# Optimization experiments

Measured on AMD Instinct MI355X. Metric: run time of the kernel, lower is better.

The kernel has to match this reference:

```python
import jax, jax.numpy as jnp
import numpy as np

LN_EPS = 1e-5

def setup_inputs() -> dict:
    key = jax.random.key(0)
    ks = jax.random.split(key, 8)
    B, d, var_dim, hidden = 1024, 32, 64, 256
    in_dim = d * var_dim
    causal_vars = jax.random.normal(ks[0], (B, d, var_dim), dtype=jnp.float32)
    adj_soft = jax.random.uniform(ks[1], (d, d), dtype=jnp.float32)
    # Per-variable MLP params (stacked along leading d axis), torch-default-like init scale
    s1 = 1.0 / np.sqrt(in_dim)
    s2 = 1.0 / np.sqrt(hidden)
    W1 = jax.random.uniform(ks[2], (d, in_dim, hidden), minval=-s1, maxval=s1, dtype=jnp.float32)
    b1 = jax.random.uniform(ks[3], (d, hidden), minval=-s1, maxval=s1, dtype=jnp.float32)
    W2 = jax.random.uniform(ks[4], (d, hidden, var_dim), minval=-s2, maxval=s2, dtype=jnp.float32)
    b2 = jax.random.uniform(ks[5], (d, var_dim), minval=-s2, maxval=s2, dtype=jnp.float32)
    gamma = jnp.ones((d, var_dim), dtype=jnp.float32)
    beta = jnp.zeros((d, var_dim), dtype=jnp.float32)
    return {"causal_vars": causal_vars, "adj_soft": adj_soft, "W1": W1, "b1": b1,
            "W2": W2, "b2": b2, "gamma": gamma, "beta": beta}

def reference(causal_vars, adj_soft, W1, b1, W2, b2, gamma, beta):
    B, d, var_dim = causal_vars.shape
    # masked parent input for equation i: adj_soft[i, j] * causal_vars[b, j, :]
    # shape (B, d_eq, d_parent, var_dim) -> flatten parents: (B, d, d*var_dim)
    x = adj_soft[None, :, :, None] * causal_vars[:, None, :, :]
    x = x.reshape(B, d, d * var_dim)
    # grouped 2-layer MLP, distinct weights per variable i
    h = jnp.einsum('bik,ikh->bih', x, W1) + b1[None]
    h = jax.nn.gelu(h, approximate=False)
    y = jnp.einsum('bih,ihv->biv', h, W2) + b2[None]
    # LayerNorm over var_dim with per-variable affine params
    mu = jnp.mean(y, axis=-1, keepdims=True)
    var = jnp.var(y, axis=-1, keepdims=True)
    y = (y - mu) * jax.lax.rsqrt(var + LN_EPS)
    return y * gamma[None] + beta[None]  # (B, d, var_dim)
```

## Files before the change

kernel.cpp:

```cpp
#include <hip/hip_runtime.h>
#include <hip/hip_bf16.h>

typedef __bf16 bf16_t;
typedef __bf16 bf16x8 __attribute__((ext_vector_type(8)));
typedef float f32x4 __attribute__((ext_vector_type(4)));

#define NB 1024
#define ND 32
#define VD 64
#define NH 256
#define NK 2048

#define OFF_A    0
#define OFF_W1T  (4u*1024u*1024u)
#define OFF_W2T  (36u*1024u*1024u)

#define GLD16(gsrc, ldst) \
  __builtin_amdgcn_global_load_lds((const __attribute__((address_space(1))) void*)(gsrc), \
                                   (__attribute__((address_space(3))) void*)(ldst), 16, 0, 0)

__global__ __launch_bounds__(256) void prep_kernel(
    const float* __restrict__ cv, const float* __restrict__ adj,
    const float* __restrict__ W1, const float* __restrict__ W2,
    bf16_t* __restrict__ A, bf16_t* __restrict__ W1T, bf16_t* __restrict__ W2T)
{
  __shared__ float Ls[64 * 67];
  int bx = blockIdx.x;
  int tid = threadIdx.x;
  if (bx < 4096) {
    int i = bx >> 7;
    int rem = bx & 127;
    int k0 = (rem >> 2) * 64;
    int h0 = (rem & 3) * 64;
    float a = adj[i * 32 + (k0 >> 6)];
    int rrow = tid >> 4, c4 = (tid & 15) * 4;
#pragma unroll
    for (int p = 0; p < 4; ++p) {
      int row = p * 16 + rrow;
      const float* src = W1 + ((size_t)(i * 2048 + k0 + row)) * 256 + h0 + c4;
      float4 v = *(const float4*)src;
#pragma unroll
      for (int j = 0; j < 4; ++j) Ls[row * 67 + c4 + j] = a * ((const float*)&v)[j];
    }
    __syncthreads();
#pragma unroll
    for (int p = 0; p < 2; ++p) {
      int u = p * 256 + tid;
      int h = u >> 3, c8 = u & 7;
      bf16x8 o;
#pragma unroll
      for (int j = 0; j < 8; ++j) o[j] = (bf16_t)Ls[(c8 * 8 + j) * 67 + h];
      *(bf16x8*)(W1T + ((size_t)(i * 256 + h0 + h)) * 2048 + k0 + c8 * 8) = o;
    }
  } else if (bx < 5120) {
    int t = (bx - 4096) * 256 + tid;
    const float4* s = (const float4*)cv + (size_t)t * 2;
    float4 v0 = s[0], v1 = s[1];
    bf16x8 o;
    o[0] = (bf16_t)v0.x; o[1] = (bf16_t)v0.y; o[2] = (bf16_t)v0.z; o[3] = (bf16_t)v0.w;
    o[4] = (bf16_t)v1.x; o[5] = (bf16_t)v1.y; o[6] = (bf16_t)v1.z; o[7] = (bf16_t)v1.w;
    *(bf16x8*)(A + (size_t)t * 8) = o;
  } else {
    int t = (bx - 5120) * 256 + tid;
    int i = t >> 11;
    int rem = t & 2047;
    int h8 = rem >> 6;
    int v = rem & 63;
    const float* src = W2 + ((size_t)(i * 256 + h8 * 8)) * 64 + v;
    bf16x8 o;
#pragma unroll
    for (int r = 0; r < 8; ++r) o[r] = (bf16_t)src[(size_t)r * 64];
    *(bf16x8*)(W2T + ((size_t)(i * 64 + v)) * 256 + h8 * 8) = o;
  }
}

__global__ __launch_bounds__(1024, 4) void sem_main_kernel(
    const bf16_t* __restrict__ A, const bf16_t* __restrict__ W1T,
    const bf16_t* __restrict__ W2T,
    const float* __restrict__ b1, const float* __restrict__ b2,
    const float* __restrict__ gamma, const float* __restrict__ beta,
    float* __restrict__ out)
{
  __shared__ char smem[73728];

  int p = blockIdx.x;
  int L = (p & 7) * 32 + (p >> 3);
  int i = L >> 3;
  int brow = (L & 7) * 128;

  int tid = threadIdx.x;
  int lane = tid & 63;
  int wid = tid >> 6;
  int wr = wid >> 2;
  int wc = wid & 3;
  int lhi = lane >> 4;
  int llo = lane & 15;

  const bf16_t* W1Ti = W1T + (size_t)i * 256 * 2048;

  int srow = tid >> 2, sc4 = tid & 3;
  int scz = sc4 ^ ((srow >> 1) & 3);
  const bf16_t* bSrc = W1Ti + (size_t)srow * 2048 + scz * 8;
  const bf16_t* aSrc = A + (size_t)(brow + srow) * 2048 + scz * 8;
  int ldsW = wid * 1024;

  auto stage = [&](int b, int kt) {
    char* base = smem + b * 24576;
    if (wid < 8) GLD16(aSrc + (size_t)kt * 32, base + ldsW);
    GLD16(bSrc + (size_t)kt * 32, base + 8192 + ldsW);
  };

  int aOff[2], bOff[4];
#pragma unroll
  for (int m = 0; m < 2; ++m) {
    int row = wr * 32 + m * 16 + llo;
    aOff[m] = row * 64 + ((lhi ^ ((row >> 1) & 3)) * 16);
  }
#pragma unroll
  for (int n = 0; n < 4; ++n) {
    int row = wc * 64 + n * 16 + llo;
    bOff[n] = 8192 + row * 64 + ((lhi ^ ((row >> 1) & 3)) * 16);
  }

  f32x4 acc[2][4];
#pragma unroll
  for (int m = 0; m < 2; ++m)
#pragma unroll
    for (int n = 0; n < 4; ++n) acc[m][n] = (f32x4){0.f, 0.f, 0.f, 0.f};

  auto compute = [&](int b) {
    const char* base = smem + b * 24576;
    bf16x8 af[2], bfr[4];
#pragma unroll
    for (int m = 0; m < 2; ++m) af[m] = *(const bf16x8*)(base + aOff[m]);
#pragma unroll
    for (int n = 0; n < 4; ++n) bfr[n] = *(const bf16x8*)(base + bOff[n]);
    __builtin_amdgcn_s_setprio(1);
#pragma unroll
    for (int m = 0; m < 2; ++m)
#pragma unroll
      for (int n = 0; n < 4; ++n)
        acc[m][n] = __builtin_amdgcn_mfma_f32_16x16x32_bf16(af[m], bfr[n], acc[m][n], 0, 0, 0);
    __builtin_amdgcn_s_setprio(0);
  };

#define WAIT_OWN_TILE() do { \
    if (wid < 8) asm volatile("s_waitcnt vmcnt(2) lgkmcnt(0)" ::: "memory"); \
    else         asm volatile("s_waitcnt vmcnt(1) lgkmcnt(0)" ::: "memory"); \
  } while (0)

  asm volatile("" ::: "memory");
  stage(0, 0); stage(1, 1);
  int bc = 0, bs = 2;
  for (int t = 0; t < 62; ++t) {
    WAIT_OWN_TILE();
    __builtin_amdgcn_s_barrier();
    asm volatile("" ::: "memory");
    stage(bs, t + 2);
    compute(bc);
    bc = (bc == 2) ? 0 : bc + 1;
    bs = (bs == 2) ? 0 : bs + 1;
  }
  WAIT_OWN_TILE();
  __builtin_amdgcn_s_barrier();
  asm volatile("" ::: "memory");
  compute(2);
  asm volatile("s_waitcnt vmcnt(0) lgkmcnt(0)" ::: "memory");
  __builtin_amdgcn_s_barrier();
  asm volatile("" ::: "memory");
  compute(0);
  __syncthreads();

  bf16_t* Hs = (bf16_t*)smem;
  float bias[4];
#pragma unroll
  for (int n = 0; n < 4; ++n) bias[n] = b1[i * 256 + wc * 64 + n * 16 + llo];
#pragma unroll
  for (int m = 0; m < 2; ++m) {
#pragma unroll
    for (int n = 0; n < 4; ++n) {
      int col = wc * 64 + n * 16 + llo;
#pragma unroll
      for (int r = 0; r < 4; ++r) {
        int row = wr * 32 + m * 16 + lhi * 4 + r;
        float x = acc[m][n][r] + bias[n];
        float gl = 0.5f * x * (1.0f + erff(x * 0.70710678118654752f));
        Hs[row * 264 + col] = (bf16_t)gl;
      }
    }
  }
  __syncthreads();

  if (wid < 8) {
    f32x4 acc2[4];
#pragma unroll
    for (int n = 0; n < 4; ++n) acc2[n] = (f32x4){0.f, 0.f, 0.f, 0.f};
    const bf16_t* W2Ti = W2T + (size_t)i * 64 * 256;
#pragma unroll
    for (int kk = 0; kk < 8; ++kk) {
      int k = kk * 32 + lhi * 8;
      bf16x8 af = *(const bf16x8*)(Hs + (wid * 16 + llo) * 264 + k);
#pragma unroll
      for (int n = 0; n < 4; ++n) {
        bf16x8 bfr = *(const bf16x8*)(W2Ti + (size_t)(n * 16 + llo) * 256 + k);
        acc2[n] = __builtin_amdgcn_mfma_f32_16x16x32_bf16(af, bfr, acc2[n], 0, 0, 0);
      }
    }
    float b2v[4], gam[4], bet[4];
#pragma unroll
    for (int n = 0; n < 4; ++n) {
      int v = n * 16 + llo;
      b2v[n] = b2[i * 64 + v];
      gam[n] = gamma[i * 64 + v];
      bet[n] = beta[i * 64 + v];
    }
#pragma unroll
    for (int r = 0; r < 4; ++r) {
      float yv[4], s = 0.f, sq = 0.f;
#pragma unroll
      for (int n = 0; n < 4; ++n) {
        yv[n] = acc2[n][r] + b2v[n];
        s += yv[n];
        sq += yv[n] * yv[n];
      }
#pragma unroll
      for (int off = 1; off < 16; off <<= 1) {
        s += __shfl_xor(s, off, 64);
        sq += __shfl_xor(sq, off, 64);
      }
      float mu = s * (1.0f / 64.0f);
      float var = sq * (1.0f / 64.0f) - mu * mu;
      float rstd = rsqrtf(var + 1e-5f);
      int row = brow + wid * 16 + lhi * 4 + r;
      float* op = out + ((size_t)row * 32 + i) * 64;
#pragma unroll
      for (int n = 0; n < 4; ++n)
        op[n * 16 + llo] = (yv[n] - mu) * rstd * gam[n] + bet[n];
    }
  }
}

extern "C" void kernel_launch(void* const* d_in, const int* in_sizes, int n_in,
                              void* d_out, int out_size, void* d_ws, size_t ws_size,
                              hipStream_t stream) {
  const float* cv    = (const float*)d_in[0];
  const float* adj   = (const float*)d_in[1];
  const float* W1    = (const float*)d_in[2];
  const float* b1    = (const float*)d_in[3];
  const float* W2    = (const float*)d_in[4];
  const float* b2    = (const float*)d_in[5];
  const float* gamma = (const float*)d_in[6];
  const float* beta  = (const float*)d_in[7];
  float* out = (float*)d_out;

  bf16_t* Abf  = (bf16_t*)((char*)d_ws + OFF_A);
  bf16_t* W1T  = (bf16_t*)((char*)d_ws + OFF_W1T);
  bf16_t* W2T  = (bf16_t*)((char*)d_ws + OFF_W2T);

  prep_kernel<<<5376, 256, 0, stream>>>(cv, adj, W1, W2, Abf, W1T, W2T);
  sem_main_kernel<<<256, 1024, 0, stream>>>(Abf, W1T, W2T, b1, b2, gamma, beta, out);
}
```

Before: 70.77 us.

## Split first GEMM along K across two blocks and reduce in fused epilogue kernel

The first GEMM now splits the K dimension in two halves, launching 512 blocks instead of 256 so more CUs have work. Each block writes bf16 partial sums to a workspace buffer. A second kernel adds the partials, applies bias and GELU, then runs the second GEMM and LayerNorm. This trades an extra kernel launch, extra global traffic and bf16 rounding of the partials for better occupancy. The old fused path is kept as a fallback when the workspace is too small.

Result: slower. 83.92 us (+18.6%).

```diff
diff --git a/kernel.cpp b/kernel.cpp
--- a/kernel.cpp
+++ b/kernel.cpp
@@ -14,6 +14,8 @@
 #define OFF_A    0
 #define OFF_W1T  (4u*1024u*1024u)
 #define OFF_W2T  (36u*1024u*1024u)
+#define OFF_HP   (37u*1024u*1024u)
+#define WS_NEED  (37ull*1024ull*1024ull + 2ull*1024ull*32ull*256ull*2ull)
 
 #define GLD16(gsrc, ldst) \
   __builtin_amdgcn_global_load_lds((const __attribute__((address_space(1))) void*)(gsrc), \
@@ -74,7 +76,204 @@
   }
 }
 
-__global__ __launch_bounds__(1024, 4) void sem_main_kernel(
+__global__ __launch_bounds__(1024, 8) void sem_gemm1_split(
+    const bf16_t* __restrict__ A, const bf16_t* __restrict__ W1T,
+    bf16_t* __restrict__ hp)
+{
+  __shared__ char smem[73728];
+
+  int p = blockIdx.x;
+  int L = (p & 7) * 64 + (p >> 3);
+  int i = L >> 4;
+  int mb = (L >> 1) & 7;
+  int ks = L & 1;
+  int brow = mb * 128;
+  int kbase = ks * 32;
+
+  int tid = threadIdx.x;
+  int lane = tid & 63;
+  int wid = tid >> 6;
+  int wr = wid >> 2;
+  int wc = wid & 3;
+  int lhi = lane >> 4;
+  int llo = lane & 15;
+
+  const bf16_t* W1Ti = W1T + (size_t)i * 256 * 2048;
+
+  int srow = tid >> 2, sc4 = tid & 3;
+  int scz = sc4 ^ ((srow >> 1) & 3);
+  const bf16_t* bSrc = W1Ti + (size_t)srow * 2048 + scz * 8;
+  const bf16_t* aSrc = A + (size_t)(brow + srow) * 2048 + scz * 8;
+  int ldsW = wid * 1024;
+
+  auto stage = [&](int b, int t) {
+    char* base = smem + b * 24576;
+    size_t ko = (size_t)(kbase + t) * 32;
+    if (wid < 8) GLD16(aSrc + ko, base + ldsW);
+    GLD16(bSrc + ko, base + 8192 + ldsW);
+  };
+
+  int aOff[2], bOff[4];
+#pragma unroll
+  for (int m = 0; m < 2; ++m) {
+    int row = wr * 32 + m * 16 + llo;
+    aOff[m] = row * 64 + ((lhi ^ ((row >> 1) & 3)) * 16);
+  }
+#pragma unroll
+  for (int n = 0; n < 4; ++n) {
+    int row = wc * 64 + n * 16 + llo;
+    bOff[n] = 8192 + row * 64 + ((lhi ^ ((row >> 1) & 3)) * 16);
+  }
+
+  f32x4 acc[2][4];
+#pragma unroll
+  for (int m = 0; m < 2; ++m)
+#pragma unroll
+    for (int n = 0; n < 4; ++n) acc[m][n] = (f32x4){0.f, 0.f, 0.f, 0.f};
+
+  auto compute = [&](int b) {
+    const char* base = smem + b * 24576;
+    bf16x8 af[2], bfr[4];
+#pragma unroll
+    for (int m = 0; m < 2; ++m) af[m] = *(const bf16x8*)(base + aOff[m]);
+#pragma unroll
+    for (int n = 0; n < 4; ++n) bfr[n] = *(const bf16x8*)(base + bOff[n]);
+    __builtin_amdgcn_s_setprio(1);
+#pragma unroll
+    for (int m = 0; m < 2; ++m)
+#pragma unroll
+      for (int n = 0; n < 4; ++n)
+        acc[m][n] = __builtin_amdgcn_mfma_f32_16x16x32_bf16(af[m], bfr[n], acc[m][n], 0, 0, 0);
+    __builtin_amdgcn_s_setprio(0);
+  };
+
+#define WAIT_OWN_TILE() do { \
+    if (wid < 8) asm volatile("s_waitcnt vmcnt(2) lgkmcnt(0)" ::: "memory"); \
+    else         asm volatile("s_waitcnt vmcnt(1) lgkmcnt(0)" ::: "memory"); \
+  } while (0)
+
+  asm volatile("" ::: "memory");
+  stage(0, 0); stage(1, 1);
+  int bc = 0, bs = 2;
+  for (int t = 0; t < 30; ++t) {
+    WAIT_OWN_TILE();
+    __builtin_amdgcn_s_barrier();
+    asm volatile("" ::: "memory");
+    stage(bs, t + 2);
+    compute(bc);
+    bc = (bc == 2) ? 0 : bc + 1;
+    bs = (bs == 2) ? 0 : bs + 1;
+  }
+  WAIT_OWN_TILE();
+  __builtin_amdgcn_s_barrier();
+  asm volatile("" ::: "memory");
+  compute(0);
+  asm volatile("s_waitcnt vmcnt(0) lgkmcnt(0)" ::: "memory");
+  __builtin_amdgcn_s_barrier();
+  asm volatile("" ::: "memory");
+  compute(1);
+
+#pragma unroll
+  for (int m = 0; m < 2; ++m) {
+#pragma unroll
+    for (int n = 0; n < 4; ++n) {
+      int col = wc * 64 + n * 16 + llo;
+#pragma unroll
+      for (int r = 0; r < 4; ++r) {
+        int row = brow + wr * 32 + m * 16 + lhi * 4 + r;
+        hp[((size_t)(ks * 1024 + row) * 32 + i) * 256 + col] = (bf16_t)acc[m][n][r];
+      }
+    }
+  }
+}
+
+__global__ __launch_bounds__(512, 2) void sem_reduce_fused(
+    const bf16_t* __restrict__ hp, const bf16_t* __restrict__ W2T,
+    const float* __restrict__ b1, const float* __restrict__ b2,
+    const float* __restrict__ gamma, const float* __restrict__ beta,
+    float* __restrict__ out)
+{
+  __shared__ char smem[67584];
+  int p = blockIdx.x;
+  int i = p & 31;
+  int brow = (p >> 5) * 128;
+
+  int tid = threadIdx.x;
+  int lane = tid & 63;
+  int wid = tid >> 6;
+  int lhi = lane >> 4;
+  int llo = lane & 15;
+
+  bf16_t* Hs = (bf16_t*)smem;
+#pragma unroll
+  for (int it = 0; it < 8; ++it) {
+    int idx = it * 512 + tid;
+    int row = idx >> 5;
+    int col = (idx & 31) * 8;
+    size_t o0 = ((size_t)(brow + row) * 32 + i) * 256 + col;
+    size_t o1 = ((size_t)(1024 + brow + row) * 32 + i) * 256 + col;
+    bf16x8 h0 = *(const bf16x8*)(hp + o0);
+    bf16x8 h1 = *(const bf16x8*)(hp + o1);
+    const float* bp = b1 + i * 256 + col;
+    bf16x8 o;
+#pragma unroll
+    for (int j = 0; j < 8; ++j) {
+      float x = (float)h0[j] + (float)h1[j] + bp[j];
+      o[j] = (bf16_t)(0.5f * x * (1.0f + erff(x * 0.70710678118654752f)));
+    }
+    *(bf16x8*)(Hs + row * 264 + col) = o;
+  }
+  __syncthreads();
+
+  f32x4 acc2[4];
+#pragma unroll
+  for (int n = 0; n < 4; ++n) acc2[n] = (f32x4){0.f, 0.f, 0.f, 0.f};
+  const bf16_t* W2Ti = W2T + (size_t)i * 64 * 256;
+#pragma unroll
+  for (int kk = 0; kk < 8; ++kk) {
+    int k = kk * 32 + lhi * 8;
+    bf16x8 af = *(const bf16x8*)(Hs + (wid * 16 + llo) * 264 + k);
+#pragma unroll
+    for (int n = 0; n < 4; ++n) {
+      bf16x8 bfr = *(const bf16x8*)(W2Ti + (size_t)(n * 16 + llo) * 256 + k);
+      acc2[n] = __builtin_amdgcn_mfma_f32_16x16x32_bf16(af, bfr, acc2[n], 0, 0, 0);
+    }
+  }
+
+  float b2v[4], gam[4], bet[4];
+#pragma unroll
+  for (int n = 0; n < 4; ++n) {
+    int v = n * 16 + llo;
+    b2v[n] = b2[i * 64 + v];
+    gam[n] = gamma[i * 64 + v];
+    bet[n] = beta[i * 64 + v];
+  }
+#pragma unroll
+  for (int r = 0; r < 4; ++r) {
+    float yv[4], s = 0.f, sq = 0.f;
+#pragma unroll
+    for (int n = 0; n < 4; ++n) {
+      yv[n] = acc2[n][r] + b2v[n];
+      s += yv[n];
+      sq += yv[n] * yv[n];
+    }
+#pragma unroll
+    for (int off = 1; off < 16; off <<= 1) {
+      s += __shfl_xor(s, off, 64);
+      sq += __shfl_xor(sq, off, 64);
+    }
+    float mu = s * (1.0f / 64.0f);
+    float var = sq * (1.0f / 64.0f) - mu * mu;
+    float rstd = rsqrtf(var + 1e-5f);
+    int row = brow + wid * 16 + lhi * 4 + r;
+    float* op = out + ((size_t)row * 32 + i) * 64;
+#pragma unroll
+    for (int n = 0; n < 4; ++n)
+      op[n * 16 + llo] = (yv[n] - mu) * rstd * gam[n] + bet[n];
+  }
+}
+
+__global__ __launch_bounds__(1024, 4) void sem_main_fused(
     const bf16_t* __restrict__ A, const bf16_t* __restrict__ W1T,
     const bf16_t* __restrict__ W2T,
     const float* __restrict__ b1, const float* __restrict__ b2,
@@ -82,7 +281,6 @@
     float* __restrict__ out)
 {
   __shared__ char smem[73728];
-
   int p = blockIdx.x;
   int L = (p & 7) * 32 + (p >> 3);
   int i = L >> 3;
@@ -97,7 +295,6 @@
   int llo = lane & 15;
 
   const bf16_t* W1Ti = W1T + (size_t)i * 256 * 2048;
-
   int srow = tid >> 2, sc4 = tid & 3;
   int scz = sc4 ^ ((srow >> 1) & 3);
   const bf16_t* bSrc = W1Ti + (size_t)srow * 2048 + scz * 8;
@@ -144,7 +341,7 @@
     __builtin_amdgcn_s_setprio(0);
   };
 
-#define WAIT_OWN_TILE() do { \
+#define WAIT_OWN_TILE_F() do { \
     if (wid < 8) asm volatile("s_waitcnt vmcnt(2) lgkmcnt(0)" ::: "memory"); \
     else         asm volatile("s_waitcnt vmcnt(1) lgkmcnt(0)" ::: "memory"); \
   } while (0)
@@ -153,7 +350,7 @@
   stage(0, 0); stage(1, 1);
   int bc = 0, bs = 2;
   for (int t = 0; t < 62; ++t) {
-    WAIT_OWN_TILE();
+    WAIT_OWN_TILE_F();
     __builtin_amdgcn_s_barrier();
     asm volatile("" ::: "memory");
     stage(bs, t + 2);
@@ -161,7 +358,7 @@
     bc = (bc == 2) ? 0 : bc + 1;
     bs = (bs == 2) ? 0 : bs + 1;
   }
-  WAIT_OWN_TILE();
+  WAIT_OWN_TILE_F();
   __builtin_amdgcn_s_barrier();
   asm volatile("" ::: "memory");
   compute(2);
@@ -256,7 +453,13 @@
   bf16_t* Abf  = (bf16_t*)((char*)d_ws + OFF_A);
   bf16_t* W1T  = (bf16_t*)((char*)d_ws + OFF_W1T);
   bf16_t* W2T  = (bf16_t*)((char*)d_ws + OFF_W2T);
+  bf16_t* hp   = (bf16_t*)((char*)d_ws + OFF_HP);
 
   prep_kernel<<<5376, 256, 0, stream>>>(cv, adj, W1, W2, Abf, W1T, W2T);
-  sem_main_kernel<<<256, 1024, 0, stream>>>(Abf, W1T, W2T, b1, b2, gamma, beta, out);
+  if (ws_size >= WS_NEED) {
+    sem_gemm1_split<<<512, 1024, 0, stream>>>(Abf, W1T, hp);
+    sem_reduce_fused<<<256, 512, 0, stream>>>(hp, W2T, b1, b2, gamma, beta, out);
+  } else {
+    sem_main_fused<<<256, 1024, 0, stream>>>(Abf, W1T, W2T, b1, b2, gamma, beta, out);
+  }
 }
```

## Load W1 fragments directly into registers and use fast erf approximation in GELU

Applied to the files above, without the earlier changes.

The B operand (W1T) now bypasses LDS: each wave loads its MFMA B fragments straight from global memory into registers, double-buffered across two k-steps, while only the A tile is still staged through LDS with a triple buffer and manual vmcnt waits. GELU's erff is replaced by the Abramowitz–Stegun polynomial plus __expf. The aim is to cut LDS traffic and size and to make the GELU epilogue cheaper. In exchange, global loads are redundant across the wave rows that share B, register pressure rises, the hand-set waitcnt counts are fragile, and erf accuracy drops to about 1e-7 absolute error, which is below bf16 rounding.

New measurement: 154.4 us. 118% more time.

```diff
diff --git a/kernel.cpp b/kernel.cpp
--- a/kernel.cpp
+++ b/kernel.cpp
@@ -18,6 +18,17 @@
 #define GLD16(gsrc, ldst) \
   __builtin_amdgcn_global_load_lds((const __attribute__((address_space(1))) void*)(gsrc), \
                                    (__attribute__((address_space(3))) void*)(ldst), 16, 0, 0)
+
+__device__ __forceinline__ float gelu_erf(float x) {
+  float z = x * 0.70710678118654752f;
+  float az = fabsf(z);
+  float t = 1.0f / (1.0f + 0.3275911f * az);
+  float p = t * (0.254829592f + t * (-0.284496736f + t * (1.421413741f +
+            t * (-1.453152027f + t * 1.061405429f))));
+  float e = __expf(-az * az);
+  float er = copysignf(1.0f - p * e, z);
+  return 0.5f * x * (1.0f + er);
+}
 
 __global__ __launch_bounds__(256) void prep_kernel(
     const float* __restrict__ cv, const float* __restrict__ adj,
@@ -81,7 +92,7 @@
     const float* __restrict__ gamma, const float* __restrict__ beta,
     float* __restrict__ out)
 {
-  __shared__ char smem[73728];
+  __shared__ char smem[67584];
 
   int p = blockIdx.x;
   int L = (p & 7) * 32 + (p >> 3);
@@ -100,27 +111,27 @@
 
   int srow = tid >> 2, sc4 = tid & 3;
   int scz = sc4 ^ ((srow >> 1) & 3);
-  const bf16_t* bSrc = W1Ti + (size_t)srow * 2048 + scz * 8;
   const bf16_t* aSrc = A + (size_t)(brow + srow) * 2048 + scz * 8;
   int ldsW = wid * 1024;
 
-  auto stage = [&](int b, int kt) {
-    char* base = smem + b * 24576;
-    if (wid < 8) GLD16(aSrc + (size_t)kt * 32, base + ldsW);
-    GLD16(bSrc + (size_t)kt * 32, base + 8192 + ldsW);
+  auto stageA = [&](int b, int kt) {
+    if (wid < 8) GLD16(aSrc + (size_t)kt * 32, smem + b * 8192 + ldsW);
   };
 
-  int aOff[2], bOff[4];
+  const bf16_t* bP = W1Ti + (size_t)(wc * 64 + llo) * 2048 + lhi * 8;
+#define LOADB(D, KT) do { \
+    D##0 = *(const bf16x8*)(bP + (size_t)(KT) * 32); \
+    D##1 = *(const bf16x8*)(bP + (size_t)(KT) * 32 + 32768); \
+    D##2 = *(const bf16x8*)(bP + (size_t)(KT) * 32 + 65536); \
+    D##3 = *(const bf16x8*)(bP + (size_t)(KT) * 32 + 98304); \
+  } while (0)
+
+  int aOff[2];
 #pragma unroll
   for (int m = 0; m < 2; ++m) {
     int row = wr * 32 + m * 16 + llo;
     aOff[m] = row * 64 + ((lhi ^ ((row >> 1) & 3)) * 16);
   }
-#pragma unroll
-  for (int n = 0; n < 4; ++n) {
-    int row = wc * 64 + n * 16 + llo;
-    bOff[n] = 8192 + row * 64 + ((lhi ^ ((row >> 1) & 3)) * 16);
-  }
 
   f32x4 acc[2][4];
 #pragma unroll
@@ -128,47 +139,55 @@
 #pragma unroll
     for (int n = 0; n < 4; ++n) acc[m][n] = (f32x4){0.f, 0.f, 0.f, 0.f};
 
-  auto compute = [&](int b) {
-    const char* base = smem + b * 24576;
-    bf16x8 af[2], bfr[4];
-#pragma unroll
-    for (int m = 0; m < 2; ++m) af[m] = *(const bf16x8*)(base + aOff[m]);
-#pragma unroll
-    for (int n = 0; n < 4; ++n) bfr[n] = *(const bf16x8*)(base + bOff[n]);
-    __builtin_amdgcn_s_setprio(1);
-#pragma unroll
-    for (int m = 0; m < 2; ++m)
-#pragma unroll
-      for (int n = 0; n < 4; ++n)
-        acc[m][n] = __builtin_amdgcn_mfma_f32_16x16x32_bf16(af[m], bfr[n], acc[m][n], 0, 0, 0);
-    __builtin_amdgcn_s_setprio(0);
-  };
-
-#define WAIT_OWN_TILE() do { \
-    if (wid < 8) asm volatile("s_waitcnt vmcnt(2) lgkmcnt(0)" ::: "memory"); \
-    else         asm volatile("s_waitcnt vmcnt(1) lgkmcnt(0)" ::: "memory"); \
+#define COMPUTE(BUF, B0, B1, B2, B3) do { \
+    const char* _ab = smem + (BUF) * 8192; \
+    bf16x8 _a0 = *(const bf16x8*)(_ab + aOff[0]); \
+    bf16x8 _a1 = *(const bf16x8*)(_ab + aOff[1]); \
+    __builtin_amdgcn_s_setprio(1); \
+    acc[0][0] = __builtin_amdgcn_mfma_f32_16x16x32_bf16(_a0, B0, acc[0][0], 0, 0, 0); \
+    acc[0][1] = __builtin_amdgcn_mfma_f32_16x16x32_bf16(_a0, B1, acc[0][1], 0, 0, 0); \
+    acc[0][2] = __builtin_amdgcn_mfma_f32_16x16x32_bf16(_a0, B2, acc[0][2], 0, 0, 0); \
+    acc[0][3] = __builtin_amdgcn_mfma_f32_16x16x32_bf16(_a0, B3, acc[0][3], 0, 0, 0); \
+    acc[1][0] = __builtin_amdgcn_mfma_f32_16x16x32_bf16(_a1, B0, acc[1][0], 0, 0, 0); \
+    acc[1][1] = __builtin_amdgcn_mfma_f32_16x16x32_bf16(_a1, B1, acc[1][1], 0, 0, 0); \
+    acc[1][2] = __builtin_amdgcn_mfma_f32_16x16x32_bf16(_a1, B2, acc[1][2], 0, 0, 0); \
+    acc[1][3] = __builtin_amdgcn_mfma_f32_16x16x32_bf16(_a1, B3, acc[1][3], 0, 0, 0); \
+    __builtin_amdgcn_s_setprio(0); \
   } while (0)
 
+#define WAITA() do { \
+    if (wid < 8) asm volatile("s_waitcnt vmcnt(9)" ::: "memory"); \
+  } while (0)
+
+  bf16x8 bA0, bA1, bA2, bA3, bB0, bB1, bB2, bB3;
+
   asm volatile("" ::: "memory");
-  stage(0, 0); stage(1, 1);
-  int bc = 0, bs = 2;
-  for (int t = 0; t < 62; ++t) {
-    WAIT_OWN_TILE();
+  stageA(0, 0); stageA(1, 1);
+  LOADB(bA, 0); LOADB(bB, 1);
+
+  for (int t = 0; t < 62; t += 2) {
+    int be = t % 3, bo = (t + 1) % 3, bn = (t + 2) % 3, bn2 = (t + 3) % 3;
+    WAITA();
     __builtin_amdgcn_s_barrier();
     asm volatile("" ::: "memory");
-    stage(bs, t + 2);
-    compute(bc);
-    bc = (bc == 2) ? 0 : bc + 1;
-    bs = (bs == 2) ? 0 : bs + 1;
-  }
-  WAIT_OWN_TILE();
+    stageA(bn, t + 2);
+    COMPUTE(be, bA0, bA1, bA2, bA3);
+    if (t + 2 < 64) LOADB(bA, t + 2);
+    WAITA();
+    __builtin_amdgcn_s_barrier();
+    asm volatile("" ::: "memory");
+    if (t + 3 < 64) stageA(bn2, t + 3);
+    COMPUTE(bo, bB0, bB1, bB2, bB3);
+    if (t + 3 < 64) LOADB(bB, t + 3);
+  }
+  WAITA();
   __builtin_amdgcn_s_barrier();
   asm volatile("" ::: "memory");
-  compute(2);
-  asm volatile("s_waitcnt vmcnt(0) lgkmcnt(0)" ::: "memory");
+  COMPUTE(62 % 3, bA0, bA1, bA2, bA3);
+  if (wid < 8) asm volatile("s_waitcnt vmcnt(4)" ::: "memory");
   __builtin_amdgcn_s_barrier();
   asm volatile("" ::: "memory");
-  compute(0);
+  COMPUTE(63 % 3, bB0, bB1, bB2, bB3);
   __syncthreads();
 
   bf16_t* Hs = (bf16_t*)smem;
@@ -183,9 +202,7 @@
 #pragma unroll
       for (int r = 0; r < 4; ++r) {
         int row = wr * 32 + m * 16 + lhi * 4 + r;
-        float x = acc[m][n][r] + bias[n];
-        float gl = 0.5f * x * (1.0f + erff(x * 0.70710678118654752f));
-        Hs[row * 264 + col] = (bf16_t)gl;
+        Hs[row * 264 + col] = (bf16_t)gelu_erf(acc[m][n][r] + bias[n]);
       }
     }
   }
```
